# Optimization experiments

Hardware: AMD Instinct MI355X
Metric: run time of the kernel (lower is better)

The kernel has to match this reference:

```python
import jax, jax.numpy as jnp
import numpy as np
from jax import lax

B, S, C, L = 256, 30, 62, 169   # batch, timesteps, channels(nodes), data_seg
OG, OH = 64, 64                 # out_gcn, out_gru
K1, K2, K3 = 64, 32, 14         # depthwise kernel sizes (169-63-31-13 = 62 = C)


def setup_inputs() -> dict:
    key = jax.random.key(0)
    ks = jax.random.split(key, 26)
    def n(k, shape, s=0.05):
        return jax.random.normal(k, shape, dtype=jnp.float32) * s
    inp = {
        "x": jax.random.normal(ks[0], (B, S, C, L), dtype=jnp.float32),
        "adj": jax.random.normal(ks[1], (C, C), dtype=jnp.float32),
        # depthwise-separable conv 1 (kernel 64)
        "dw1_w": n(ks[2], (C, 1, K1)), "dw1_b": n(ks[3], (C,)),
        "pw1_w": n(ks[4], (C, C, 1)), "pw1_b": n(ks[5], (C,)),
        # depthwise-separable conv 2 (kernel 32)
        "dw2_w": n(ks[6], (C, 1, K2)), "dw2_b": n(ks[7], (C,)),
        "pw2_w": n(ks[8], (C, C, 1)), "pw2_b": n(ks[9], (C,)),
        # depthwise-separable conv 3 (kernel 14)
        "dw3_w": n(ks[10], (C, 1, K3)), "dw3_b": n(ks[11], (C,)),
        "pw3_w": n(ks[12], (C, C, 1)), "pw3_b": n(ks[13], (C,)),
        # GraphConvolution(data_seg, out_gcn): support = x @ W; out = adj @ support + b
        "gcn_w": n(ks[14], (L, OG)), "gcn_b": n(ks[15], (OG,)),
        # GRU-style gate Linears (out_gcn+out_gru -> out_gru), torch layout (out, in)
        "Wr_w": n(ks[16], (OH, OG + OH)), "Wr_b": n(ks[17], (OH,)),
        "Wu_w": n(ks[18], (OH, OG + OH)), "Wu_b": n(ks[19], (OH,)),
        "Wc_w": n(ks[20], (OH, OG + OH)), "Wc_b": n(ks[21], (OH,)),
        # extra learned gate biases b_r/b_u/b_c (init zeros in torch)
        "b_r": jnp.zeros((OH,), jnp.float32),
        "b_u": jnp.zeros((OH,), jnp.float32),
        "b_c": jnp.zeros((OH,), jnp.float32),
    }
    return inp


def _dsconv(x, dw, dwb, pw, pwb):
    # x: (b, c, l); depthwise (groups=c, valid padding) then pointwise 1x1
    dn = ("NCH", "OIH", "NCH")
    y = lax.conv_general_dilated(x, dw, (1,), "VALID", dimension_numbers=dn,
                                 feature_group_count=x.shape[1]) + dwb[None, :, None]
    y = lax.conv_general_dilated(y, pw, (1,), "VALID", dimension_numbers=dn) + pwb[None, :, None]
    return y


def reference(x, adj, dw1_w, dw1_b, pw1_w, pw1_b, dw2_w, dw2_b, pw2_w, pw2_b,
              dw3_w, dw3_b, pw3_w, pw3_b, gcn_w, gcn_b,
              Wr_w, Wr_b, Wu_w, Wu_b, Wc_w, Wc_b, b_r, b_u, b_c):
    b, s, c, l = x.shape
    oh = b_r.shape[0]

    def step(h, xt):            # h: (b*c, oh), xt: (b, c, l)
        d = _dsconv(xt, dw1_w, dw1_b, pw1_w, pw1_b)
        d = _dsconv(d, dw2_w, dw2_b, pw2_w, pw2_b)
        d = _dsconv(d, dw3_w, dw3_b, pw3_w, pw3_b)      # (b, c, c)
        adj_t = jax.nn.sigmoid(d + adj)                  # adaptive adjacency
        support = jnp.einsum("bcl,lf->bcf", xt, gcn_w)
        g = jnp.einsum("bij,bjf->bif", adj_t, support) + gcn_b  # (b, c, og)
        gf = g.reshape(b * c, -1)
        cat = jnp.concatenate([gf, h], axis=-1)
        r = jax.nn.sigmoid(cat @ Wr_w.T + Wr_b + b_r)
        u = jax.nn.sigmoid(cat @ Wu_w.T + Wu_b + b_u)
        cc = jnp.tanh(jnp.concatenate([gf, r * h], axis=-1) @ Wc_w.T + Wc_b + b_c)
        h_new = u * h + (1.0 - u) * cc
        return h_new, None

    h0 = jnp.zeros((b * c, oh), x.dtype)
    xs = jnp.swapaxes(x, 0, 1)          # (s, b, c, l)
    h_last, _ = lax.scan(step, h0, xs)
    return h_last.reshape(b, c, oh)[:, -1, :]   # (b, out_gru)
```

## Files before the change

### kernel.cpp

```cpp
#include <hip/hip_runtime.h>
#include <math.h>

#define BB 256
#define SS 30
#define CC 62
#define LL 169
#define OG 64
#define OH 64
#define KK1 64
#define KK2 32
#define KK3 14
#define FLEN 108

typedef __attribute__((ext_vector_type(8))) short s16x8;
typedef __attribute__((ext_vector_type(4))) float f32x4;

__device__ __forceinline__ unsigned short f2bf(float f) {
    unsigned u = __float_as_uint(f);
    u += 0x7fffu + ((u >> 16) & 1u);
    return (unsigned short)(u >> 16);
}
__device__ __forceinline__ float bflo(unsigned v) { return __uint_as_float(v << 16); }
__device__ __forceinline__ float bfhi(unsigned v) { return __uint_as_float(v & 0xffff0000u); }

__device__ __forceinline__ void gload_lds4(const void* g, void* l) {
    __builtin_amdgcn_global_load_lds(
        (const __attribute__((address_space(1))) void*)g,
        (__attribute__((address_space(3))) void*)l, 4, 0, 0);
}

__global__ __launch_bounds__(1024) void k_setup1(
        const float* __restrict__ dw1, const float* __restrict__ dw1b,
        const float* __restrict__ pw1, const float* __restrict__ pw1b,
        const float* __restrict__ dw2, const float* __restrict__ dw2b,
        const float* __restrict__ pw2, const float* __restrict__ pw2b,
        const float* __restrict__ dw3, const float* __restrict__ dw3b,
        const float* __restrict__ pw3, const float* __restrict__ pw3b,
        const float* __restrict__ Wr, const float* __restrict__ Wrb, const float* __restrict__ br,
        const float* __restrict__ Wu, const float* __restrict__ Wub, const float* __restrict__ bu,
        const float* __restrict__ Wc, const float* __restrict__ Wcb, const float* __restrict__ bc,
        float* __restrict__ Bmg, float* __restrict__ WtAll,
        float* __restrict__ bias192, float* __restrict__ beff) {
    __shared__ float g23[CC * KK3];
    __shared__ float Am[CC * 45];
    __shared__ float by2[CC], vals[CC];
    int tid = threadIdx.x;

    for (int idx = tid; idx < OG * 192; idx += 1024) {
        int i = idx / 192, q = idx - i * 192;
        int gate = q >> 6, f = q & 63;
        const float* W = gate == 0 ? Wr : (gate == 1 ? Wu : Wc);
        WtAll[idx] = W[f * (OG + OH) + i];
    }
    if (tid < 192) {
        int gate = tid >> 6, f = tid & 63;
        const float* Wb = gate == 0 ? Wrb : (gate == 1 ? Wub : Wcb);
        const float* bb = gate == 0 ? br  : (gate == 1 ? bu  : bc);
        bias192[tid] = Wb[f] + bb[f];
    }
    for (int idx = tid; idx < CC * KK3; idx += 1024) {
        int c1 = idx / KK3, k3 = idx - c1 * KK3;
        float s = 0.f;
        for (int c2 = 0; c2 < CC; ++c2)
            s += pw3[61 * CC + c2] * pw2[c2 * CC + c1] * dw3[c2 * KK3 + k3];
        g23[idx] = s;
    }
    if (tid < CC) {
        int c1 = tid;
        float bz1 = pw1b[c1];
        for (int c0 = 0; c0 < CC; ++c0) bz1 += pw1[c1 * CC + c0] * dw1b[c0];
        float s2 = 0.f;
        for (int k = 0; k < KK2; ++k) s2 += dw2[c1 * KK2 + k];
        by2[c1] = dw2b[c1] + bz1 * s2;
    }
    __syncthreads();
    if (tid < CC) {
        int c2 = tid;
        float bz2 = pw2b[c2];
        for (int c1 = 0; c1 < CC; ++c1) bz2 += pw2[c2 * CC + c1] * by2[c1];
        float s3 = 0.f;
        for (int k = 0; k < KK3; ++k) s3 += dw3[c2 * KK3 + k];
        vals[c2] = pw3[61 * CC + c2] * (dw3b[c2] + bz2 * s3);
    }
    for (int idx = tid; idx < CC * 45; idx += 1024) {
        int c1 = idx / 45, m = idx - c1 * 45;
        int k2lo = max(0, m - (KK3 - 1));
        int k2hi = min(KK2 - 1, m);
        float s = 0.f;
        for (int k2 = k2lo; k2 <= k2hi; ++k2)
            s += dw2[c1 * KK2 + k2] * g23[c1 * KK3 + (m - k2)];
        Am[idx] = s;
    }
    __syncthreads();
    if (tid == 0) {
        float s = pw3b[61];
        for (int c2 = 0; c2 < CC; ++c2) s += vals[c2];
        *beff = s;
    }
    for (int idx = tid; idx < CC * 45; idx += 1024) {
        int c0 = idx / 45, m = idx - c0 * 45;
        float s = 0.f;
        for (int c1 = 0; c1 < CC; ++c1) s += pw1[c1 * CC + c0] * Am[c1 * 45 + m];
        Bmg[idx] = s;
    }
}

__global__ __launch_bounds__(128) void k_setupF(
        const float* __restrict__ Bmg, const float* __restrict__ dw1,
        unsigned short* __restrict__ Ftb) {
    __shared__ float Bl[45];
    int c0 = blockIdx.x;
    int o = threadIdx.x;
    if (c0 < CC && o < 45) Bl[o] = Bmg[c0 * 45 + o];
    __syncthreads();
    if (o >= 112) return;
    float s = 0.f;
    if (c0 < CC && o < FLEN) {
        int mlo = max(0, o - (KK1 - 1));
        int mhi = min(44, o);
        for (int m = mlo; m <= mhi; ++m)
            s += Bl[m] * dw1[c0 * KK1 + (o - m)];
    }
    Ftb[o * 64 + c0] = f2bf(s);
}

__global__ __launch_bounds__(256, 2) void k_main(
        const float* __restrict__ x, const float* __restrict__ adj,
        const unsigned short* __restrict__ Ftb, const float* __restrict__ beff_p,
        float* __restrict__ wxb) {
    __shared__ __align__(16) unsigned xf32[10478];
    __shared__ __align__(16) unsigned short xT[176 * 64];
    __shared__ float dacc[4][64];
    __shared__ float adjt[CC];
    int bt = blockIdx.x;
    int tid = threadIdx.x;
    int lane = tid & 63, wid = tid >> 6;
    const float* xg = x + (size_t)bt * (CC * LL);
    unsigned* xTu = (unsigned*)xT;

    #pragma unroll
    for (int it = 0; it < 41; ++it) {
        int di = it * 256 + tid;
        if (di < 10478)
            gload_lds4((const char*)xg + (size_t)di * 4,
                       (char*)xf32 + it * 1024 + wid * 256);
    }
    float be = *beff_p;
    float arow = 0.f;
    if (tid < CC) arow = adj[61 * CC + tid];
    int col = lane & 15, rb4 = lane >> 4;
    const unsigned short* ap0 = Ftb + ((wid * 16 + col) * 64 + rb4 * 8);
    s16x8 pa0 = *(const s16x8*)ap0;
    s16x8 pa1 = *(const s16x8*)(ap0 + 32);
    ((float*)dacc)[tid] = 0.f;
    for (int i = tid; i < 169; i += 256) xTu[(i * 32 + 31) ^ ((i & 7) << 2)] = 0;
    for (int i = tid; i < 224; i += 256) {
        int r = 169 + (i >> 5), d2 = i & 31;
        xTu[(r * 32 + d2) ^ ((r & 7) << 2)] = 0;
    }
    __syncthreads();

    for (int idx = tid; idx < 31 * 169; idx += 256) {
        int l = idx / 31, cp = idx - l * 31;
        unsigned lo = xf32[(2 * cp) * 169 + l];
        unsigned hi = xf32[(2 * cp + 1) * 169 + l];
        unsigned v = (unsigned)f2bf(__uint_as_float(lo))
                   | ((unsigned)f2bf(__uint_as_float(hi)) << 16);
        xTu[(l * 32 + cp) ^ ((l & 7) << 2)] = v;
    }
    __syncthreads();

    f32x4 zacc[5];
    #pragma unroll
    for (int d = 0; d < 5; ++d) zacc[d] = (f32x4){0.f, 0.f, 0.f, 0.f};
    int kb = rb4 * 16;
    int xr = (lane & 7) << 4;
    #pragma unroll
    for (int h = 0; h < 2; ++h) {
        int mt = wid + 4 * h;
        if (mt < 7) {
            s16x8 a0, a1;
            if (h == 0) { a0 = pa0; a1 = pa1; }
            else {
                const unsigned short* ap = Ftb + ((mt * 16 + col) * 64 + rb4 * 8);
                a0 = *(const s16x8*)ap;
                a1 = *(const s16x8*)(ap + 32);
            }
            #pragma unroll
            for (int d = 0; d < 5; ++d) {
                int nt = mt + d;
                int bbyte = ((nt * 16 + col) * 128 + kb) ^ xr;
                s16x8 b0 = *(const s16x8*)((const char*)xT + bbyte);
                s16x8 b1 = *(const s16x8*)((const char*)xT + bbyte + 64);
                zacc[d] = __builtin_amdgcn_mfma_f32_16x16x32_bf16(a0, b0, zacc[d], 0, 0, 0);
                zacc[d] = __builtin_amdgcn_mfma_f32_16x16x32_bf16(a1, b1, zacc[d], 0, 0, 0);
            }
        }
    }
    int jc = col - rb4 * 4;
    #pragma unroll
    for (int d = 0; d < 5; ++d) {
        #pragma unroll
        for (int r = 0; r < 4; ++r) {
            int j = 16 * d + jc - r;
            if ((unsigned)j < 62u) atomicAdd(&dacc[rb4][j], zacc[d][r]);
        }
    }
    __syncthreads();

    if (tid < CC) {
        float dv = dacc[0][tid] + dacc[1][tid] + dacc[2][tid] + dacc[3][tid];
        adjt[tid] = 1.f / (1.f + __expf(-(dv + be + arow)));
    }
    __syncthreads();

    if (tid < 176) {
        float s = 0.f;
        if (tid < LL) {
            #pragma unroll 2
            for (int j = 0; j < CC; ++j)
                s += adjt[j] * __uint_as_float(xf32[j * LL + tid]);
        }
        wxb[(size_t)bt * 176 + tid] = s;
    }
}

__global__ __launch_bounds__(256) void k_gg(
        const float* __restrict__ wxb, const float* __restrict__ gcnw,
        const float* __restrict__ gcnb, const float* __restrict__ WtAll,
        const float* __restrict__ bias192, float* __restrict__ gates) {
    __shared__ float wxl[8 * 176];
    __shared__ float Gl[8 * 64];
    int bt0 = blockIdx.x * 8;
    int tid = threadIdx.x;
    const float* src = wxb + (size_t)bt0 * 176;
    for (int i = tid; i < 8 * 176; i += 256) wxl[i] = src[i];
    __syncthreads();
    #pragma unroll
    for (int rep = 0; rep < 2; ++rep) {
        int i = rep * 256 + tid;
        int bl = i >> 6, f = i & 63;
        float s = gcnb[f];
        const float* wr = wxl + bl * 176;
        #pragma unroll 13
        for (int l = 0; l < LL; ++l) s += wr[l] * gcnw[l * OG + f];
        Gl[i] = s;
    }
    __syncthreads();
    float* gout = gates + (size_t)bt0 * 192;
    #pragma unroll
    for (int rep = 0; rep < 6; ++rep) {
        int i = rep * 256 + tid;
        int bl = i / 192, q = i - bl * 192;
        const float* gr = Gl + bl * 64;
        float s = bias192[q];
        #pragma unroll 16
        for (int k = 0; k < OG; ++k) s += gr[k] * WtAll[k * 192 + q];
        gout[i] = s;
    }
}

__global__ __launch_bounds__(256) void k_scan(
        const float* __restrict__ gates,
        const float* __restrict__ Wr, const float* __restrict__ Wu, const float* __restrict__ Wc,
        float* __restrict__ out) {
    __shared__ float hl[OH], rhl[OH];
    int b = blockIdx.x;
    int tid = threadIdx.x;
    int f = tid >> 2, q = tid & 3;
    float wr[16], wu[16], wc[16];
    #pragma unroll
    for (int i = 0; i < 16; ++i) {
        int col = OG + q * 16 + i;
        wr[i] = Wr[f * (OG + OH) + col];
        wu[i] = Wu[f * (OG + OH) + col];
        wc[i] = Wc[f * (OG + OH) + col];
    }
    float h = 0.f;
    if (tid < OH) hl[tid] = 0.f;
    __syncthreads();
    for (int t = 0; t < SS; ++t) {
        const float* gp = gates + ((size_t)b * SS + t) * 192;
        float gr = gp[f];
        float gu = gp[64 + f];
        float gc = gp[128 + f];
        float rv = 0.f, uv = 0.f;
        #pragma unroll
        for (int i = 0; i < 16; ++i) {
            float hv = hl[q * 16 + i];
            rv += wr[i] * hv;
            uv += wu[i] * hv;
        }
        rv += __shfl_xor(rv, 1); rv += __shfl_xor(rv, 2);
        uv += __shfl_xor(uv, 1); uv += __shfl_xor(uv, 2);
        float r = 1.f / (1.f + __expf(-(rv + gr)));
        float u = 1.f / (1.f + __expf(-(uv + gu)));
        if (q == 0) rhl[f] = r * h;
        __syncthreads();
        float cv = 0.f;
        #pragma unroll
        for (int i = 0; i < 16; ++i) cv += wc[i] * rhl[q * 16 + i];
        cv += __shfl_xor(cv, 1); cv += __shfl_xor(cv, 2);
        float cc = tanhf(cv + gc);
        if (q == 0) {
            h = u * h + (1.f - u) * cc;
            hl[f] = h;
        }
        __syncthreads();
    }
    if (q == 0) out[b * OH + f] = h;
}

extern "C" void kernel_launch(void* const* d_in, const int* in_sizes, int n_in,
                              void* d_out, int out_size, void* d_ws, size_t ws_size,
                              hipStream_t stream) {
    const float* x    = (const float*)d_in[0];
    const float* adj  = (const float*)d_in[1];
    const float* dw1w = (const float*)d_in[2];
    const float* dw1b = (const float*)d_in[3];
    const float* pw1w = (const float*)d_in[4];
    const float* pw1b = (const float*)d_in[5];
    const float* dw2w = (const float*)d_in[6];
    const float* dw2b = (const float*)d_in[7];
    const float* pw2w = (const float*)d_in[8];
    const float* pw2b = (const float*)d_in[9];
    const float* dw3w = (const float*)d_in[10];
    const float* dw3b = (const float*)d_in[11];
    const float* pw3w = (const float*)d_in[12];
    const float* pw3b = (const float*)d_in[13];
    const float* gcnw = (const float*)d_in[14];
    const float* gcnb = (const float*)d_in[15];
    const float* Wrw  = (const float*)d_in[16];
    const float* Wrb  = (const float*)d_in[17];
    const float* Wuw  = (const float*)d_in[18];
    const float* Wub  = (const float*)d_in[19];
    const float* Wcw  = (const float*)d_in[20];
    const float* Wcb  = (const float*)d_in[21];
    const float* br   = (const float*)d_in[22];
    const float* bu   = (const float*)d_in[23];
    const float* bc   = (const float*)d_in[24];
    float* out = (float*)d_out;

    char* ws = (char*)d_ws;
    unsigned short* Ftb = (unsigned short*)(ws + 0);
    float* WtAll        = (float*)(ws + 14336);
    float* bias192      = (float*)(ws + 63488);
    float* beff         = (float*)(ws + 64256);
    float* Bmg          = (float*)(ws + 64320);
    float* wxb          = (float*)(ws + 76800);
    float* gates        = (float*)(ws + 5483520);
    (void)ws_size; (void)in_sizes; (void)n_in; (void)out_size;

    k_setup1<<<1, 1024, 0, stream>>>(dw1w, dw1b, pw1w, pw1b, dw2w, dw2b, pw2w, pw2b,
                                     dw3w, dw3b, pw3w, pw3b,
                                     Wrw, Wrb, br, Wuw, Wub, bu, Wcw, Wcb, bc,
                                     Bmg, WtAll, bias192, beff);
    k_setupF<<<64, 128, 0, stream>>>(Bmg, dw1w, Ftb);
    k_main<<<BB * SS, 256, 0, stream>>>(x, adj, Ftb, beff, wxb);
    k_gg<<<BB * SS / 8, 256, 0, stream>>>(wxb, gcnw, gcnb, WtAll, bias192, gates);
    k_scan<<<BB, 256, 0, stream>>>(gates, Wrw, Wuw, Wcw, out);
}
```

Baseline: 340.4 us.

## Stream x through registers into bf16 LDS tile, drop fp32 LDS staging

Removes the 42KB fp32 LDS staging buffer for x. Each thread now issues software-pipelined dwordx2 global loads into registers, converts channel pairs with v_cvt_pk_bf16_f32, and writes the swizzled bf16 transposed tile directly. This cuts LDS use so occupancy can rise from 2 to 3 blocks per CU, and it also prefetches the second A fragment and gives each wave its own atomic accumulator slots. The final adjacency-weighted sum reads the bf16 tile instead of fp32, which lowers precision in that stage.

```diff
diff --git a/kernel.cpp b/kernel.cpp
--- a/kernel.cpp
+++ b/kernel.cpp
@@ -22,12 +22,6 @@
 }
 __device__ __forceinline__ float bflo(unsigned v) { return __uint_as_float(v << 16); }
 __device__ __forceinline__ float bfhi(unsigned v) { return __uint_as_float(v & 0xffff0000u); }
-
-__device__ __forceinline__ void gload_lds4(const void* g, void* l) {
-    __builtin_amdgcn_global_load_lds(
-        (const __attribute__((address_space(1))) void*)g,
-        (__attribute__((address_space(3))) void*)l, 4, 0, 0);
-}
 
 __global__ __launch_bounds__(1024) void k_setup1(
         const float* __restrict__ dw1, const float* __restrict__ dw1b,
@@ -124,50 +118,82 @@
     Ftb[o * 64 + c0] = f2bf(s);
 }
 
-__global__ __launch_bounds__(256, 2) void k_main(
+#define STG_ISSUE(i, s) do {                                                   \
+    const float* pA = xg + 338 * cpa[i] + l0a[i];                              \
+    const float* pB = pA + 169;                                                \
+    asm volatile("global_load_dwordx2 %0, %1, off" : "=v"(A0[s]) : "v"(pA));   \
+    asm volatile("global_load_dwordx2 %0, %1, off" : "=v"(A1[s]) : "v"(pA + 2));\
+    asm volatile("global_load_dwordx2 %0, %1, off" : "=v"(B0[s]) : "v"(pB));   \
+    asm volatile("global_load_dwordx2 %0, %1, off" : "=v"(B1[s]) : "v"(pB + 2));\
+} while (0)
+
+#define STG_CONSUME(i, s, VM) do {                                             \
+    asm volatile("s_waitcnt vmcnt(" VM ")"                                     \
+        : "+v"(A0[s]), "+v"(A1[s]), "+v"(B0[s]), "+v"(B1[s]));                 \
+    unsigned d0, d1, d2, d3;                                                   \
+    asm("v_cvt_pk_bf16_f32 %0, %1, %2" : "=v"(d0)                             \
+        : "v"(__uint_as_float(A0[s].x)), "v"(__uint_as_float(B0[s].x)));       \
+    asm("v_cvt_pk_bf16_f32 %0, %1, %2" : "=v"(d1)                             \
+        : "v"(__uint_as_float(A0[s].y)), "v"(__uint_as_float(B0[s].y)));       \
+    asm("v_cvt_pk_bf16_f32 %0, %1, %2" : "=v"(d2)                             \
+        : "v"(__uint_as_float(A1[s].x)), "v"(__uint_as_float(B1[s].x)));       \
+    asm("v_cvt_pk_bf16_f32 %0, %1, %2" : "=v"(d3)                             \
+        : "v"(__uint_as_float(A1[s].y)), "v"(__uint_as_float(B1[s].y)));       \
+    int l0 = l0a[i], cp = cpa[i];                                              \
+    xTu[((l0 + 0) * 32 + cp) ^ (((l0 + 0) & 7) << 2)] = d0;                    \
+    xTu[((l0 + 1) * 32 + cp) ^ (((l0 + 1) & 7) << 2)] = d1;                    \
+    xTu[((l0 + 2) * 32 + cp) ^ (((l0 + 2) & 7) << 2)] = d2;                    \
+    xTu[((l0 + 3) * 32 + cp) ^ (((l0 + 3) & 7) << 2)] = d3;                    \
+} while (0)
+
+__global__ __launch_bounds__(256, 3) void k_main(
         const float* __restrict__ x, const float* __restrict__ adj,
         const unsigned short* __restrict__ Ftb, const float* __restrict__ beff_p,
         float* __restrict__ wxb) {
-    __shared__ __align__(16) unsigned xf32[10478];
     __shared__ __align__(16) unsigned short xT[176 * 64];
-    __shared__ float dacc[4][64];
-    __shared__ float adjt[CC];
+    __shared__ float dacc[4][4][64];
+    __shared__ float adjt[64];
     int bt = blockIdx.x;
     int tid = threadIdx.x;
     int lane = tid & 63, wid = tid >> 6;
+    int col = lane & 15, rb4 = lane >> 4;
+    unsigned* xTu = (unsigned*)xT;
     const float* xg = x + (size_t)bt * (CC * LL);
-    unsigned* xTu = (unsigned*)xT;
-
-    #pragma unroll
-    for (int it = 0; it < 41; ++it) {
-        int di = it * 256 + tid;
-        if (di < 10478)
-            gload_lds4((const char*)xg + (size_t)di * 4,
-                       (char*)xf32 + it * 1024 + wid * 256);
-    }
+
     float be = *beff_p;
-    float arow = 0.f;
-    if (tid < CC) arow = adj[61 * CC + tid];
-    int col = lane & 15, rb4 = lane >> 4;
+    float arow = (tid < CC) ? adj[61 * CC + tid] : 0.f;
     const unsigned short* ap0 = Ftb + ((wid * 16 + col) * 64 + rb4 * 8);
     s16x8 pa0 = *(const s16x8*)ap0;
     s16x8 pa1 = *(const s16x8*)(ap0 + 32);
-    ((float*)dacc)[tid] = 0.f;
+    int mt2c = wid + 4 < 7 ? wid + 4 : 6;
+    const unsigned short* ap1 = Ftb + ((mt2c * 16 + col) * 64 + rb4 * 8);
+    s16x8 pb0 = *(const s16x8*)ap1;
+    s16x8 pb1 = *(const s16x8*)(ap1 + 32);
+    __builtin_amdgcn_sched_barrier(0);
+
+    uint2 A0[3], A1[3], B0[3], B1[3];
+    int l0a[6], cpa[6];
+    #pragma unroll
+    for (int i = 0; i < 6; ++i) {
+        int w = tid + i * 256; if (w > 1332) w = 1332;
+        int lg = w / 31; cpa[i] = w - lg * 31;
+        l0a[i] = (lg < 42) ? 4 * lg : 165;
+    }
+    STG_ISSUE(0, 0); STG_ISSUE(1, 1); STG_ISSUE(2, 2);
     for (int i = tid; i < 169; i += 256) xTu[(i * 32 + 31) ^ ((i & 7) << 2)] = 0;
     for (int i = tid; i < 224; i += 256) {
-        int r = 169 + (i >> 5), d2 = i & 31;
-        xTu[(r * 32 + d2) ^ ((r & 7) << 2)] = 0;
-    }
-    __syncthreads();
-
-    for (int idx = tid; idx < 31 * 169; idx += 256) {
-        int l = idx / 31, cp = idx - l * 31;
-        unsigned lo = xf32[(2 * cp) * 169 + l];
-        unsigned hi = xf32[(2 * cp + 1) * 169 + l];
-        unsigned v = (unsigned)f2bf(__uint_as_float(lo))
-                   | ((unsigned)f2bf(__uint_as_float(hi)) << 16);
-        xTu[(l * 32 + cp) ^ ((l & 7) << 2)] = v;
-    }
+        int r = 169 + (i >> 5), dd = i & 31;
+        xTu[(r * 32 + dd) ^ ((r & 7) << 2)] = 0;
+    }
+    ((float*)dacc)[tid] = 0.f;       ((float*)dacc)[tid + 256] = 0.f;
+    ((float*)dacc)[tid + 512] = 0.f; ((float*)dacc)[tid + 768] = 0.f;
+
+    STG_CONSUME(0, 0, "8"); STG_ISSUE(3, 0);
+    STG_CONSUME(1, 1, "8"); STG_ISSUE(4, 1);
+    STG_CONSUME(2, 2, "8"); STG_ISSUE(5, 2);
+    STG_CONSUME(3, 0, "8");
+    STG_CONSUME(4, 1, "4");
+    STG_CONSUME(5, 2, "0");
     __syncthreads();
 
     f32x4 zacc[5];
@@ -179,13 +205,8 @@
     for (int h = 0; h < 2; ++h) {
         int mt = wid + 4 * h;
         if (mt < 7) {
-            s16x8 a0, a1;
-            if (h == 0) { a0 = pa0; a1 = pa1; }
-            else {
-                const unsigned short* ap = Ftb + ((mt * 16 + col) * 64 + rb4 * 8);
-                a0 = *(const s16x8*)ap;
-                a1 = *(const s16x8*)(ap + 32);
-            }
+            s16x8 a0 = h == 0 ? pa0 : pb0;
+            s16x8 a1 = h == 0 ? pa1 : pb1;
             #pragma unroll
             for (int d = 0; d < 5; ++d) {
                 int nt = mt + d;
@@ -203,13 +224,17 @@
         #pragma unroll
         for (int r = 0; r < 4; ++r) {
             int j = 16 * d + jc - r;
-            if ((unsigned)j < 62u) atomicAdd(&dacc[rb4][j], zacc[d][r]);
+            if ((unsigned)j < 62u) atomicAdd(&dacc[wid][rb4][j], zacc[d][r]);
         }
     }
     __syncthreads();
 
     if (tid < CC) {
-        float dv = dacc[0][tid] + dacc[1][tid] + dacc[2][tid] + dacc[3][tid];
+        float dv = 0.f;
+        #pragma unroll
+        for (int w = 0; w < 4; ++w)
+            #pragma unroll
+            for (int g = 0; g < 4; ++g) dv += dacc[w][g][tid];
         adjt[tid] = 1.f / (1.f + __expf(-(dv + be + arow)));
     }
     __syncthreads();
@@ -217,9 +242,14 @@
     if (tid < 176) {
         float s = 0.f;
         if (tid < LL) {
-            #pragma unroll 2
-            for (int j = 0; j < CC; ++j)
-                s += adjt[j] * __uint_as_float(xf32[j * LL + tid]);
+            int xorv = (tid & 7) << 2;
+            int m0 = tid % 31;
+            #pragma unroll
+            for (int mm = 0; mm < 31; ++mm) {
+                int m = m0 + mm; if (m >= 31) m -= 31;
+                unsigned v = xTu[(tid * 32 + m) ^ xorv];
+                s += adjt[2 * m] * bflo(v) + adjt[2 * m + 1] * bfhi(v);
+            }
         }
         wxb[(size_t)bt * 176 + tid] = s;
     }
```

Result: faster. 291.8 us (-14.3%).
